# Optimization experiments

Measured on AMD Instinct MI355X. Metric: run time of the kernel, lower is better.

## Reference

```python
import jax, jax.numpy as jnp
import numpy as np

# Hyperparameters matching init_kwargs
IN_CH = 64
OUT_CH = 128
KERNEL = (3, 3)
STRIDE = (1, 1)
PADDING = 'SAME'
K_ORDER = 3          # spline order
G_INTERVALS = 3      # grid intervals
GRID_MIN, GRID_MAX = -1.0, 1.0
N_BASIS = G_INTERVALS + K_ORDER  # basis functions per input = 6
PATCH_DIM = IN_CH * KERNEL[0] * KERNEL[1]  # 576


def _grid():
    # Extended uniform knot vector: G + 2k + 1 knots
    h = (GRID_MAX - GRID_MIN) / G_INTERVALS
    return jnp.arange(-K_ORDER, G_INTERVALS + K_ORDER + 1, dtype=jnp.float32) * h + GRID_MIN


def _b_splines(x):
    # x: [N, n_in] -> bases: [N, n_in, G + k]
    grid = _grid()  # [G + 2k + 1]
    xe = x[..., None]  # [N, n_in, 1]
    bases = ((xe >= grid[:-1]) & (xe < grid[1:])).astype(x.dtype)  # order-0, [N, n_in, G+2k]
    for p in range(1, K_ORDER + 1):
        left = (xe - grid[: -(p + 1)]) / (grid[p:-1] - grid[: -(p + 1)]) * bases[..., :-1]
        right = (grid[p + 1:] - xe) / (grid[p + 1:] - grid[1:-p]) * bases[..., 1:]
        bases = left + right
    return bases  # [N, n_in, G + k]


def setup_inputs() -> dict:
    key = jax.random.key(0)
    k0, k1, k2, k3 = jax.random.split(key, 4)
    x = jax.random.normal(k0, (8, 64, 64, IN_CH), dtype=jnp.float32)
    base_w = jax.random.normal(k1, (OUT_CH, PATCH_DIM), dtype=jnp.float32) * 0.05
    spline_w = jax.random.normal(k2, (OUT_CH, PATCH_DIM, N_BASIS), dtype=jnp.float32) * 0.05
    bias = jax.random.normal(k3, (OUT_CH,), dtype=jnp.float32) * 0.05
    return {'x': x, 'base_w': base_w, 'spline_w': spline_w, 'bias': bias}


def reference(x, base_w, spline_w, bias):
    batch = x.shape[0]
    dn = ('NHWC', 'HWIO', 'NHWC')
    patches = jax.lax.conv_general_dilated_patches(
        lhs=x, filter_shape=KERNEL, window_strides=STRIDE, padding=PADDING,
        dimension_numbers=dn)  # [B, H, W, patch_dim]
    out_spatial = patches.shape[1:-1]
    p = patches.reshape(-1, PATCH_DIM)  # [N, patch_dim]
    # EfficientKAN: residual (silu) branch + spline branch + bias
    base_out = jax.nn.silu(p) @ base_w.T                      # [N, out]
    bases = _b_splines(p)                                      # [N, patch_dim, G+k]
    spline_out = jnp.einsum('nig,oig->no', bases, spline_w)    # [N, out]
    y = base_out + spline_out + bias
    return y.reshape(batch, *out_spatial, OUT_CH)
```

## Files before the change

### kernel.cpp

```cpp
#include <hip/hip_runtime.h>

typedef __attribute__((ext_vector_type(8))) short short8;
typedef __attribute__((ext_vector_type(16))) float f32x16;

#define FT2_SHORTS (512u * 4356u * 8u)
#define PLANE16    4356

typedef __attribute__((address_space(3))) unsigned int lds_u32_t;
typedef __attribute__((address_space(1))) const unsigned int g_u32_t;

__device__ __forceinline__ unsigned short f2bf(float x) {
    union { float f; unsigned u; } v; v.f = x;
    unsigned r = v.u + 0x7FFFu + ((v.u >> 16) & 1u);
    return (unsigned short)(r >> 16);
}

__device__ __forceinline__ void feat8(float p, unsigned short* uf) {
    float e   = __expf(-p);
    float sig = 1.f / (1.f + e);
    uf[0] = f2bf(p * sig);
    float u  = p * 1.5f + 4.5f;
    float fj = floorf(u);
    int   j0 = (int)fj;
    float t  = u - fj;
    bool  inr = (u >= 0.f) && (u < 9.f);
    float t2 = t * t, t3 = t2 * t;
    const float c16 = 1.f / 6.f;
    float r0 = t3 * c16;
    float r1 = (-3.f * t3 + 3.f * t2 + 3.f * t + 1.f) * c16;
    float r2 = (3.f * t3 - 6.f * t2 + 4.f) * c16;
    float s1 = 1.f - t;
    float r3 = s1 * s1 * s1 * c16;
#pragma unroll
    for (int g = 0; g < 6; ++g) {
        int r = j0 - g;
        float v = (r == 0) ? r0 : ((r == 1) ? r1 : ((r == 2) ? r2 : ((r == 3) ? r3 : 0.f)));
        uf[1 + g] = f2bf(inr ? v : 0.f);
    }
    uf[7] = 0;
}

__global__ void prep_w(const float* __restrict__ bw, const float* __restrict__ sw,
                       unsigned short* __restrict__ wt) {
    int idx = blockIdx.x * 256 + threadIdx.x;
    if (idx >= 128 * 576) return;
    int o = idx / 576;
    int i = idx - o * 576;
    int slab = i >> 3, e = i & 7;
    int ch = e ^ (o & 7);
    union { unsigned short u[8]; uint4 v; } pk;
    pk.u[0] = f2bf(bw[o * 576 + i]);
    const float* s = sw + (size_t)(o * 576 + i) * 6;
#pragma unroll
    for (int f = 0; f < 6; ++f) pk.u[1 + f] = f2bf(s[f]);
    pk.u[7] = 0;
    *(uint4*)(wt + ((size_t)slab * 8192 + o * 64 + ch * 8)) = pk.v;
}

__global__ void halo_k(unsigned short* __restrict__ ft) {
    int z = blockIdx.x;
    for (int t = threadIdx.x; t < 260; t += 256) {
        int yy, xx;
        if (t < 66)       { yy = 0;       xx = t; }
        else if (t < 132) { yy = 65;      xx = t - 66; }
        else if (t < 196) { yy = t - 131; xx = 0; }
        else              { yy = t - 195; xx = 65; }
        short8 pad = { 0, 0, (short)0x3CAB, (short)0x3EF5,
                       (short)0x3EF5, (short)0x3CAB, 0, 0 };
        ((short8*)ft)[z * PLANE16 + yy * 66 + xx] = pad;
    }
}

__global__ __launch_bounds__(256)
void feat_k(const float* __restrict__ x, unsigned short* __restrict__ ft) {
    __shared__ float Xl[64 * 65];
    const int line = blockIdx.x;
    const int b = line >> 6, y = line & 63;
    const float* xl = x + (size_t)line * 4096;
    const int tid = threadIdx.x;
    for (int f4 = tid; f4 < 1024; f4 += 256) {
        float4 v = ((const float4*)xl)[f4];
        int xx = f4 >> 4, c4 = (f4 & 15) << 2;
        float* d = &Xl[xx * 65 + c4];
        d[0] = v.x; d[1] = v.y; d[2] = v.z; d[3] = v.w;
    }
    __syncthreads();
    const int xx = tid & 63;
    const int cw = tid >> 6;
#pragma unroll 4
    for (int p = 0; p < 16; ++p) {
        int c = cw + (p << 2);
        float pv = Xl[xx * 65 + c];
        union { unsigned short u[8]; uint4 v; } pk;
        feat8(pv, pk.u);
        size_t o16 = (size_t)(c * 8 + b) * PLANE16 + (y + 1) * 66 + (xx + 1);
        *(uint4*)(ft + (o16 << 3)) = pk.v;
    }
}

#define STAGE(itn)                                                               \
    {                                                                            \
        const unsigned short* ssrc = wt + (size_t)(itn) * 8192 + stoff;          \
        unsigned short* sdst = &Bs[((itn) & 1) ? 8192 : 0] + stoff;              \
        _Pragma("unroll")                                                        \
        for (int j = 0; j < 4; ++j)                                              \
            __builtin_amdgcn_global_load_lds((g_u32_t*)(ssrc + j * 2048),        \
                                             (lds_u32_t*)(sdst + j * 2048), 16, 0, 0); \
    }

#define ALOAD(itn, ADST)                                                         \
    _Pragma("unroll")                                                            \
    for (int s_ = 0; s_ < 4; ++s_) {                                             \
        int i_  = (itn) * 8 + s_ * 2 + h;                                        \
        int c_  = (i_ * 7282) >> 16;                                             \
        int i9_ = i_ - c_ * 9;                                                   \
        int kh_ = (i9_ * 11) >> 5;                                               \
        int kw_ = i9_ - kh_ * 3;                                                 \
        int t16 = c_ * (8 * PLANE16) + kh_ * 66 + kw_ + abase;                   \
        ADST[2 * s_]     = fptr[t16];                                            \
        ADST[2 * s_ + 1] = fptr[t16 + 32];                                       \
    }

#define KSTEP(s_, ACUR)                                                          \
    {                                                                            \
        short8 bf0 = *(const short8*)(bsrd + roff0 + ((((s_) * 2 + h) ^ swb) << 4)); \
        short8 bf1 = *(const short8*)(bsrd + roff1 + ((((s_) * 2 + h) ^ swb) << 4)); \
        acc00 = __builtin_amdgcn_mfma_f32_32x32x16_bf16(ACUR[2*(s_)],   bf0, acc00, 0, 0, 0); \
        acc01 = __builtin_amdgcn_mfma_f32_32x32x16_bf16(ACUR[2*(s_)],   bf1, acc01, 0, 0, 0); \
        acc10 = __builtin_amdgcn_mfma_f32_32x32x16_bf16(ACUR[2*(s_)+1], bf0, acc10, 0, 0, 0); \
        acc11 = __builtin_amdgcn_mfma_f32_32x32x16_bf16(ACUR[2*(s_)+1], bf1, acc11, 0, 0, 0); \
    }

__global__ __launch_bounds__(256, 1)
void convkan_gemm(const unsigned short* __restrict__ ft,
                  const unsigned short* __restrict__ wt,
                  const float* __restrict__ bias,
                  float* __restrict__ out) {
    __shared__ unsigned short Bs[2 * 8192];

    const int tid  = threadIdx.x;
    const int blk  = blockIdx.x;
    const int lane = tid & 63;
    const int wave = tid >> 6;
    const int g    = wave >> 1;
    const int ni   = wave & 1;
    const int l32  = lane & 31;
    const int h    = lane >> 5;

    const int b  = blk >> 5;
    const int h0 = (blk & 31) << 1;
    const int abase = b * PLANE16 + (h0 + g) * 66 + l32;
    const short8* fptr = (const short8*)ft;

    const int stoff = wave * 512 + lane * 8;

    const int roff0 = (ni * 64 + l32) * 128;
    const int roff1 = roff0 + 32 * 128;
    const int swb   = l32 & 7;

    f32x16 acc00, acc01, acc10, acc11;
#pragma unroll
    for (int e = 0; e < 16; ++e) { acc00[e] = 0.f; acc01[e] = 0.f; acc10[e] = 0.f; acc11[e] = 0.f; }

    short8 aA[8], aB[8];
    STAGE(0);
    ALOAD(0, aA);

    for (int it = 0; it < 72; it += 2) {
        __syncthreads();
        STAGE(it + 1);
        ALOAD(it + 1, aB);
        {
            const char* bsrd = (const char*)Bs;
            KSTEP(0, aA) KSTEP(1, aA) KSTEP(2, aA) KSTEP(3, aA)
        }
        __syncthreads();
        if (it + 2 < 72) {
            STAGE(it + 2);
            ALOAD(it + 2, aA);
        }
        {
            const char* bsrd = (const char*)Bs + 16384;
            KSTEP(0, aB) KSTEP(1, aB) KSTEP(2, aB) KSTEP(3, aB)
        }
    }

    const float bv0 = bias[ni * 64 + l32];
    const float bv1 = bias[ni * 64 + 32 + l32];
    const int mrow0 = blk * 128 + g * 64 + h * 4;
    float* o0 = out + (size_t)mrow0 * 128 + ni * 64 + l32;
#pragma unroll
    for (int r = 0; r < 16; ++r) {
        int row = (r & 3) + ((r >> 2) << 3);
        o0[(size_t)row * 128]             = acc00[r] + bv0;
        o0[(size_t)row * 128 + 32]        = acc01[r] + bv1;
        o0[(size_t)(row + 32) * 128]      = acc10[r] + bv0;
        o0[(size_t)(row + 32) * 128 + 32] = acc11[r] + bv1;
    }
}

extern "C" void kernel_launch(void* const* d_in, const int* in_sizes, int n_in,
                              void* d_out, int out_size, void* d_ws, size_t ws_size,
                              hipStream_t stream) {
    (void)in_sizes; (void)n_in; (void)out_size; (void)ws_size;
    const float* x        = (const float*)d_in[0];
    const float* base_w   = (const float*)d_in[1];
    const float* spline_w = (const float*)d_in[2];
    const float* bias     = (const float*)d_in[3];
    float* out = (float*)d_out;

    unsigned short* ft = (unsigned short*)d_ws;
    unsigned short* wt = ft + FT2_SHORTS;

    hipLaunchKernelGGL(prep_w, dim3((128 * 576 + 255) / 256), dim3(256), 0, stream,
                       base_w, spline_w, wt);
    hipLaunchKernelGGL(halo_k, dim3(512), dim3(256), 0, stream, ft);
    hipLaunchKernelGGL(feat_k, dim3(512), dim3(256), 0, stream, x, ft);
    hipLaunchKernelGGL(convkan_gemm, dim3(256), dim3(256), 0, stream,
                       ft, wt, bias, out);
}
```

Before: 159.6 us.

## Fuse prep kernels into one launch and halve GEMM tile to 64 rows

Merges the weight-packing, halo-padding and feature-expansion kernels into a single prep kernel, with 144 threads per block doing the weight packing. This cuts two kernel launches and their gaps. The GEMM now gives each block one output row of 64 pixels instead of two rows of 128, with each wave owning 32 output channels. The grid grows from 256 to 512 blocks with two blocks per CU allowed, which raises occupancy and balances work across CUs. The cost is that each block reloads the full weight slab for half as many rows, so weight traffic per output doubles and MFMA reuse of each B fragment falls.

```diff
diff --git a/kernel.cpp b/kernel.cpp
--- a/kernel.cpp
+++ b/kernel.cpp
@@ -40,44 +40,44 @@
     uf[7] = 0;
 }
 
-__global__ void prep_w(const float* __restrict__ bw, const float* __restrict__ sw,
-                       unsigned short* __restrict__ wt) {
-    int idx = blockIdx.x * 256 + threadIdx.x;
-    if (idx >= 128 * 576) return;
-    int o = idx / 576;
-    int i = idx - o * 576;
-    int slab = i >> 3, e = i & 7;
-    int ch = e ^ (o & 7);
-    union { unsigned short u[8]; uint4 v; } pk;
-    pk.u[0] = f2bf(bw[o * 576 + i]);
-    const float* s = sw + (size_t)(o * 576 + i) * 6;
-#pragma unroll
-    for (int f = 0; f < 6; ++f) pk.u[1 + f] = f2bf(s[f]);
-    pk.u[7] = 0;
-    *(uint4*)(wt + ((size_t)slab * 8192 + o * 64 + ch * 8)) = pk.v;
-}
-
-__global__ void halo_k(unsigned short* __restrict__ ft) {
-    int z = blockIdx.x;
-    for (int t = threadIdx.x; t < 260; t += 256) {
-        int yy, xx;
-        if (t < 66)       { yy = 0;       xx = t; }
-        else if (t < 132) { yy = 65;      xx = t - 66; }
-        else if (t < 196) { yy = t - 131; xx = 0; }
-        else              { yy = t - 195; xx = 65; }
+__global__ __launch_bounds__(256)
+void prep_all(const float* __restrict__ x,
+              const float* __restrict__ bw, const float* __restrict__ sw,
+              unsigned short* __restrict__ ft, unsigned short* __restrict__ wt) {
+    const int blk = blockIdx.x;
+    const int tid = threadIdx.x;
+
+    if (tid < 144) {
+        int idx = blk * 144 + tid;
+        int o = idx / 576;
+        int i = idx - o * 576;
+        int slab = i >> 3, e = i & 7;
+        int ch = e ^ (o & 7);
+        union { unsigned short u[8]; uint4 v; } pk;
+        pk.u[0] = f2bf(bw[o * 576 + i]);
+        const float* s = sw + (size_t)(o * 576 + i) * 6;
+#pragma unroll
+        for (int f = 0; f < 6; ++f) pk.u[1 + f] = f2bf(s[f]);
+        pk.u[7] = 0;
+        *(uint4*)(wt + ((size_t)slab * 8192 + o * 64 + ch * 8)) = pk.v;
+    }
+
+    {
         short8 pad = { 0, 0, (short)0x3CAB, (short)0x3EF5,
                        (short)0x3EF5, (short)0x3CAB, 0, 0 };
-        ((short8*)ft)[z * PLANE16 + yy * 66 + xx] = pad;
-    }
-}
-
-__global__ __launch_bounds__(256)
-void feat_k(const float* __restrict__ x, unsigned short* __restrict__ ft) {
+        for (int t = tid; t < 260; t += 256) {
+            int yy, xx;
+            if (t < 66)       { yy = 0;       xx = t; }
+            else if (t < 132) { yy = 65;      xx = t - 66; }
+            else if (t < 196) { yy = t - 131; xx = 0; }
+            else              { yy = t - 195; xx = 65; }
+            ((short8*)ft)[blk * PLANE16 + yy * 66 + xx] = pad;
+        }
+    }
+
     __shared__ float Xl[64 * 65];
-    const int line = blockIdx.x;
-    const int b = line >> 6, y = line & 63;
-    const float* xl = x + (size_t)line * 4096;
-    const int tid = threadIdx.x;
+    const int b = blk >> 6, y = blk & 63;
+    const float* xl = x + (size_t)blk * 4096;
     for (int f4 = tid; f4 < 1024; f4 += 256) {
         float4 v = ((const float4*)xl)[f4];
         int xx = f4 >> 4, c4 = (f4 & 15) << 2;
@@ -123,15 +123,12 @@
 
 #define KSTEP(s_, ACUR)                                                          \
     {                                                                            \
-        short8 bf0 = *(const short8*)(bsrd + roff0 + ((((s_) * 2 + h) ^ swb) << 4)); \
-        short8 bf1 = *(const short8*)(bsrd + roff1 + ((((s_) * 2 + h) ^ swb) << 4)); \
-        acc00 = __builtin_amdgcn_mfma_f32_32x32x16_bf16(ACUR[2*(s_)],   bf0, acc00, 0, 0, 0); \
-        acc01 = __builtin_amdgcn_mfma_f32_32x32x16_bf16(ACUR[2*(s_)],   bf1, acc01, 0, 0, 0); \
-        acc10 = __builtin_amdgcn_mfma_f32_32x32x16_bf16(ACUR[2*(s_)+1], bf0, acc10, 0, 0, 0); \
-        acc11 = __builtin_amdgcn_mfma_f32_32x32x16_bf16(ACUR[2*(s_)+1], bf1, acc11, 0, 0, 0); \
-    }
-
-__global__ __launch_bounds__(256, 1)
+        short8 bf = *(const short8*)(bsrd + roff + ((((s_) * 2 + h) ^ swb) << 4)); \
+        acc0 = __builtin_amdgcn_mfma_f32_32x32x16_bf16(ACUR[2*(s_)],   bf, acc0, 0, 0, 0); \
+        acc1 = __builtin_amdgcn_mfma_f32_32x32x16_bf16(ACUR[2*(s_)+1], bf, acc1, 0, 0, 0); \
+    }
+
+__global__ __launch_bounds__(256, 2)
 void convkan_gemm(const unsigned short* __restrict__ ft,
                   const unsigned short* __restrict__ wt,
                   const float* __restrict__ bias,
@@ -142,25 +139,22 @@
     const int blk  = blockIdx.x;
     const int lane = tid & 63;
     const int wave = tid >> 6;
-    const int g    = wave >> 1;
-    const int ni   = wave & 1;
     const int l32  = lane & 31;
     const int h    = lane >> 5;
 
-    const int b  = blk >> 5;
-    const int h0 = (blk & 31) << 1;
-    const int abase = b * PLANE16 + (h0 + g) * 66 + l32;
+    const int b = blk >> 6;
+    const int y = blk & 63;
+    const int abase = b * PLANE16 + y * 66 + l32;
     const short8* fptr = (const short8*)ft;
 
     const int stoff = wave * 512 + lane * 8;
 
-    const int roff0 = (ni * 64 + l32) * 128;
-    const int roff1 = roff0 + 32 * 128;
-    const int swb   = l32 & 7;
-
-    f32x16 acc00, acc01, acc10, acc11;
-#pragma unroll
-    for (int e = 0; e < 16; ++e) { acc00[e] = 0.f; acc01[e] = 0.f; acc10[e] = 0.f; acc11[e] = 0.f; }
+    const int roff = (wave * 32 + l32) * 128;
+    const int swb  = l32 & 7;
+
+    f32x16 acc0, acc1;
+#pragma unroll
+    for (int e = 0; e < 16; ++e) { acc0[e] = 0.f; acc1[e] = 0.f; }
 
     short8 aA[8], aB[8];
     STAGE(0);
@@ -185,17 +179,14 @@
         }
     }
 
-    const float bv0 = bias[ni * 64 + l32];
-    const float bv1 = bias[ni * 64 + 32 + l32];
-    const int mrow0 = blk * 128 + g * 64 + h * 4;
-    float* o0 = out + (size_t)mrow0 * 128 + ni * 64 + l32;
+    const float bv = bias[wave * 32 + l32];
+    const int mrow0 = blk * 64 + h * 4;
+    float* o0 = out + (size_t)mrow0 * 128 + wave * 32 + l32;
 #pragma unroll
     for (int r = 0; r < 16; ++r) {
         int row = (r & 3) + ((r >> 2) << 3);
-        o0[(size_t)row * 128]             = acc00[r] + bv0;
-        o0[(size_t)row * 128 + 32]        = acc01[r] + bv1;
-        o0[(size_t)(row + 32) * 128]      = acc10[r] + bv0;
-        o0[(size_t)(row + 32) * 128 + 32] = acc11[r] + bv1;
+        o0[(size_t)row * 128]        = acc0[r] + bv;
+        o0[(size_t)(row + 32) * 128] = acc1[r] + bv;
     }
 }
 
@@ -212,10 +203,8 @@
     unsigned short* ft = (unsigned short*)d_ws;
     unsigned short* wt = ft + FT2_SHORTS;
 
-    hipLaunchKernelGGL(prep_w, dim3((128 * 576 + 255) / 256), dim3(256), 0, stream,
-                       base_w, spline_w, wt);
-    hipLaunchKernelGGL(halo_k, dim3(512), dim3(256), 0, stream, ft);
-    hipLaunchKernelGGL(feat_k, dim3(512), dim3(256), 0, stream, x, ft);
-    hipLaunchKernelGGL(convkan_gemm, dim3(256), dim3(256), 0, stream,
+    hipLaunchKernelGGL(prep_all, dim3(512), dim3(256), 0, stream,
+                       x, base_w, spline_w, ft, wt);
+    hipLaunchKernelGGL(convkan_gemm, dim3(512), dim3(256), 0, stream,
                        ft, wt, bias, out);
 }
```

After: 167.1 us. +4.7%, slower.
